# Kernel tuning notes

Hardware: AMD Instinct MI355X
Metric: run time of the kernel (lower is better)

Reference implementation:

```python
import jax, jax.numpy as jnp
import numpy as np

K = 5          # k = min(5, min(S, T)) with S = T = 4096
SIGMA = 1.0
EPS_VAR = 1e-08
EPS_LOG = 1e-08


def _entropy(p):
    # sum(-p * log2(clamp(p, 1e-8)), axis=1).mean()
    return jnp.sum(-p * jnp.log2(jnp.clip(p, EPS_LOG, None)), axis=1).mean()


def _pairwise_dist(x):
    # Euclidean cdist via GEMM (matches torch's use_mm_for_euclid path)
    sq = jnp.sum(x * x, axis=1)                       # [N]
    d2 = sq[:, None] + sq[None, :] - 2.0 * (x @ x.T)  # [N, N]
    d2 = jnp.maximum(d2, 0.0)
    # safe sqrt (zero diagonal) — value identical, grad-safe
    return jnp.where(d2 > 0, jnp.sqrt(jnp.where(d2 > 0, d2, 1.0)), 0.0)


def _row_var(block):
    # sqrt(k-th smallest distance per row + eps): max of k smallest
    kth = -jax.lax.top_k(-block, K)[0][:, -1]
    return jnp.sqrt(kth + EPS_VAR)                    # [rows]


def _sim(block, var_row, zero_diag):
    s = jnp.exp(-block / (2.0 * (var_row[:, None] * SIGMA) ** 2))
    if zero_diag:
        n = block.shape[0]
        s = s * (1.0 - jnp.eye(n, dtype=s.dtype))
    return s


def _forward(Feature_all, logit_all, y_source):
    S = y_source.shape[0]
    logit_source = logit_all[:S]
    logit_target = logit_all[S:]

    # cross-entropy on source
    logp = jax.nn.log_softmax(logit_source, axis=1)
    loss_cl = -jnp.take_along_axis(logp, y_source[:, None], axis=1).mean()

    # entropy of target softmax
    loss_ce = _entropy(jax.nn.softmax(logit_target, axis=1))

    # reg_loss_dist
    dist = _pairwise_dist(Feature_all)                # [N, N]
    d_ss = dist[:S, :S]
    d_st = dist[:S, S:]
    d_tt = dist[S:, S:]
    d_ts = dist[S:, :S]

    sim_ss = _sim(d_ss, _row_var(d_ss), True)
    sim_st = _sim(d_st, _row_var(d_st), False)
    sim_tt = _sim(d_tt, _row_var(d_tt), True)
    sim_ts = _sim(d_ts, _row_var(d_ts), False)

    src_intra = jnp.max(sim_ss, axis=1)
    src_inter = jnp.max(sim_st, axis=1)
    tgt_intra = jnp.max(sim_tt, axis=1)
    tgt_inter = jnp.max(sim_ts, axis=1)

    loss_reg = (jnp.abs(src_intra - src_inter).mean()
                + jnp.abs(tgt_intra - tgt_inter).mean())
    return loss_cl, loss_ce, loss_reg


def setup_inputs() -> dict:
    key = jax.random.key(0)
    k1, k2, k3 = jax.random.split(key, 3)
    N, D, C, S = 8192, 256, 65, 4096
    return {
        "Feature_all": jax.random.normal(k1, (N, D), dtype=jnp.float32),
        "logit_all": jax.random.normal(k2, (N, C), dtype=jnp.float32),
        "y_source": jax.random.randint(k3, (S,), 0, C, dtype=jnp.int64
                                       if jax.config.jax_enable_x64 else jnp.int32),
        "device": 0,
    }


def reference(Feature_all, logit_all, y_source, device):
    del device  # torch-specific, ignored
    return _forward(Feature_all, logit_all, y_source)
```

## Files before the change

### kernel.cpp

```cpp
#include <hip/hip_runtime.h>
#include <stdint.h>

#define Nn 8192
#define Dd 256
#define Ss 4096
#define Cc 65

#define TI 128
#define TJ 128
#define BK 32
#define CHUNK 256
#define NCHUNK (Nn / CHUNK)
#define NJT (CHUNK / TJ)
#define KS (Dd / BK)
#define NL (NCHUNK * 2)

#define BIGF 3.0e37f

typedef float f4 __attribute__((ext_vector_type(4)));
typedef __bf16 bf8 __attribute__((ext_vector_type(8)));

__device__ __forceinline__ float wredsum(float v) {
#pragma unroll
  for (int o = 32; o; o >>= 1) v += __shfl_xor(v, o, 64);
  return v;
}
__device__ __forceinline__ float wredmax(float v) {
#pragma unroll
  for (int o = 32; o; o >>= 1) v = fmaxf(v, __shfl_xor(v, o, 64));
  return v;
}

__device__ __forceinline__ unsigned short f2bf(float f) {
  unsigned int u = __float_as_uint(f);
  u = (u + 0x7fffu + ((u >> 16) & 1u)) >> 16;
  return (unsigned short)u;
}

__global__ __launch_bounds__(256) void prep_kernel(const float* __restrict__ X,
                                                   unsigned short* __restrict__ xb,
                                                   float* __restrict__ sqn) {
  int row = blockIdx.x * 4 + (threadIdx.x >> 6);
  int lane = threadIdx.x & 63;
  f4 v = ((const f4*)(X + (size_t)row * Dd))[lane];
  float ss = v[0] * v[0] + v[1] * v[1] + v[2] * v[2] + v[3] * v[3];
  ss = wredsum(ss);
  if (lane == 0) sqn[row] = ss;
  ushort4 o;
  o.x = f2bf(v[0]); o.y = f2bf(v[1]); o.z = f2bf(v[2]); o.w = f2bf(v[3]);
  ((ushort4*)(xb + (size_t)row * Dd))[lane] = o;
}

__device__ __forceinline__ void stage16(const void* g, void* l) {
  __builtin_amdgcn_global_load_lds((__attribute__((address_space(1))) void*)g,
                                   (__attribute__((address_space(3))) void*)l, 16, 0, 0);
}

__global__ __launch_bounds__(256) void dist_kernel(const unsigned short* __restrict__ xb,
                                                   const float* __restrict__ sqn,
                                                   float* __restrict__ top5ws) {
  __shared__ unsigned short ldsA[2][TJ * BK];
  __shared__ unsigned short ldsB[2][TI * BK];

  const int tid = threadIdx.x;
  const int lane = tid & 63;
  const int wv = tid >> 6;
  const int q = lane >> 4;
  const int c = lane & 15;
  const int jw = wv & 1;
  const int iw = wv >> 1;

  const int ib = (blockIdx.x / NCHUNK) * TI;
  const int chunk = blockIdx.x % NCHUNK;
  const int jc0 = chunk * CHUNK;

  const int swz = q ^ ((lane >> 1) & 3);
  const int pr = lane >> 2;
  const int qd = (lane & 3) ^ ((lane >> 3) & 3);
  const int u0 = wv * 2, u1 = wv * 2 + 1;
  const int gcol = qd * 8;

  float top[4][5];
#pragma unroll
  for (int a = 0; a < 4; ++a)
#pragma unroll
    for (int b = 0; b < 5; ++b) top[a][b] = BIGF;

  const int iwbase = ib + iw * 64;

  for (int jt = 0; jt < NJT; ++jt) {
    const int jb = jc0 + jt * TJ;

    f4 acc[4][4];
    f4 z = {0.f, 0.f, 0.f, 0.f};
#pragma unroll
    for (int a = 0; a < 4; ++a)
#pragma unroll
      for (int b2 = 0; b2 < 4; ++b2) acc[a][b2] = z;

    stage16(xb + (size_t)(jb + u0 * 16 + pr) * Dd + gcol, &ldsA[0][u0 * 512]);
    stage16(xb + (size_t)(jb + u1 * 16 + pr) * Dd + gcol, &ldsA[0][u1 * 512]);
    stage16(xb + (size_t)(ib + u0 * 16 + pr) * Dd + gcol, &ldsB[0][u0 * 512]);
    stage16(xb + (size_t)(ib + u1 * 16 + pr) * Dd + gcol, &ldsB[0][u1 * 512]);
    __syncthreads();

#pragma unroll
    for (int ks = 0; ks < KS; ++ks) {
      const int b = ks & 1;
      if (ks + 1 < KS) {
        const int k0 = (ks + 1) * BK;
        stage16(xb + (size_t)(jb + u0 * 16 + pr) * Dd + k0 + gcol, &ldsA[b ^ 1][u0 * 512]);
        stage16(xb + (size_t)(jb + u1 * 16 + pr) * Dd + k0 + gcol, &ldsA[b ^ 1][u1 * 512]);
        stage16(xb + (size_t)(ib + u0 * 16 + pr) * Dd + k0 + gcol, &ldsB[b ^ 1][u0 * 512]);
        stage16(xb + (size_t)(ib + u1 * 16 + pr) * Dd + k0 + gcol, &ldsB[b ^ 1][u1 * 512]);
      }
      bf8 aF[4], bF[4];
#pragma unroll
      for (int rt = 0; rt < 4; ++rt)
        aF[rt] = *(const bf8*)&ldsA[b][(jw * 64 + rt * 16 + c) * 32 + swz * 8];
#pragma unroll
      for (int ct = 0; ct < 4; ++ct)
        bF[ct] = *(const bf8*)&ldsB[b][(iw * 64 + ct * 16 + c) * 32 + swz * 8];
#pragma unroll
      for (int rt = 0; rt < 4; ++rt)
#pragma unroll
        for (int ct = 0; ct < 4; ++ct)
          acc[rt][ct] = __builtin_amdgcn_mfma_f32_16x16x32_bf16(aF[rt], bF[ct], acc[rt][ct], 0, 0, 0);
      __syncthreads();
    }

    const int jrow = jb + jw * 64;
    f4 sq4[4];
#pragma unroll
    for (int rt = 0; rt < 4; ++rt) sq4[rt] = *(const f4*)&sqn[jrow + rt * 16 + q * 4];
    const bool mayDiag = (jrow == iwbase);
#pragma unroll
    for (int ct = 0; ct < 4; ++ct) {
      float t[16];
#pragma unroll
      for (int rt = 0; rt < 4; ++rt)
#pragma unroll
        for (int r = 0; r < 4; ++r)
          t[rt * 4 + r] = fmaf(acc[rt][ct][r], -2.0f, sq4[rt][r]);
      if (mayDiag && ((c >> 2) == q)) t[ct * 4 + (c & 3)] = BIGF;
      float tm = fminf(fminf(fminf(fminf(t[0], t[1]), fminf(t[2], t[3])),
                             fminf(fminf(t[4], t[5]), fminf(t[6], t[7]))),
                       fminf(fminf(fminf(t[8], t[9]), fminf(t[10], t[11])),
                             fminf(fminf(t[12], t[13]), fminf(t[14], t[15]))));
      if (tm < top[ct][4]) {
#pragma unroll
        for (int kk = 0; kk < 16; ++kk) {
          float x = t[kk];
          if (x < top[ct][4]) {
#pragma unroll
            for (int s = 0; s < 4; ++s) {
              float lo = fminf(top[ct][s], x);
              x = fmaxf(top[ct][s], x);
              top[ct][s] = lo;
            }
            top[ct][4] = x;
          }
        }
      }
    }
  }

  const int list = chunk * 2 + jw;
#pragma unroll
  for (int ct = 0; ct < 4; ++ct) {
    float a0 = top[ct][0], a1 = top[ct][1], a2 = top[ct][2], a3 = top[ct][3], a4 = top[ct][4];
#pragma unroll
    for (int off = 16; off <= 32; off <<= 1) {
      float b0 = __shfl_xor(a0, off, 64);
      float b1 = __shfl_xor(a1, off, 64);
      float b2 = __shfl_xor(a2, off, 64);
      float b3 = __shfl_xor(a3, off, 64);
      float b4 = __shfl_xor(a4, off, 64);
      float c0 = fminf(a0, b0);
      float c1 = fminf(fminf(a1, b1), fmaxf(a0, b0));
      float c2 = fminf(fminf(a2, b2), fminf(fmaxf(a1, b0), fmaxf(a0, b1)));
      float c3 = fminf(fminf(a3, b3), fminf(fmaxf(a2, b0), fminf(fmaxf(a1, b1), fmaxf(a0, b2))));
      float c4 = fminf(fminf(a4, b4),
                       fminf(fmaxf(a3, b0),
                             fminf(fmaxf(a2, b1), fminf(fmaxf(a1, b2), fmaxf(a0, b3)))));
      a0 = c0; a1 = c1; a2 = c2; a3 = c3; a4 = c4;
    }
    if (q == 0) {
      int i = iwbase + ct * 16 + c;
      top5ws[(size_t)(list * 5 + 0) * Nn + i] = a0;
      top5ws[(size_t)(list * 5 + 1) * Nn + i] = a1;
      top5ws[(size_t)(list * 5 + 2) * Nn + i] = a2;
      top5ws[(size_t)(list * 5 + 3) * Nn + i] = a3;
      top5ws[(size_t)(list * 5 + 4) * Nn + i] = a4;
    }
  }
}

__device__ __forceinline__ void merge5(const float* a, const float* b, float* o) {
  float t0 = fminf(a[0], b[0]);
  float t1 = fminf(fminf(a[1], b[1]), fmaxf(a[0], b[0]));
  float t2 = fminf(fminf(a[2], b[2]), fminf(fmaxf(a[1], b[0]), fmaxf(a[0], b[1])));
  float t3 = fminf(fminf(a[3], b[3]), fminf(fmaxf(a[2], b[0]), fminf(fmaxf(a[1], b[1]), fmaxf(a[0], b[2]))));
  float t4 = fminf(fminf(a[4], b[4]),
                   fminf(fmaxf(a[3], b[0]),
                         fminf(fmaxf(a[2], b[1]), fminf(fmaxf(a[1], b[2]), fmaxf(a[0], b[3])))));
  o[0] = t0; o[1] = t1; o[2] = t2; o[3] = t3; o[4] = t4;
}

__global__ __launch_bounds__(256) void tail_kernel(const float* __restrict__ logit,
                                                   const int* __restrict__ y,
                                                   const float* __restrict__ top5ws,
                                                   const float* __restrict__ sqn,
                                                   float* __restrict__ part_cl,
                                                   float* __restrict__ part_ce,
                                                   float* __restrict__ part_reg) {
  __shared__ float red[256];
  const int bx = blockIdx.x;
  if (bx < 2048) {
    int row = bx * 4 + (threadIdx.x >> 6);
    int lane = threadIdx.x & 63;
    const float* xr = logit + (size_t)row * Cc;
    float x1 = xr[lane];
    float x2 = (lane == 0) ? xr[64] : -BIGF;
    float mx = wredmax(fmaxf(x1, x2));
    float e1 = expf(x1 - mx);
    float e2 = (lane == 0) ? expf(x2 - mx) : 0.f;
    float Z = wredsum(e1 + e2);
    float res;
    if (row < Ss) {
      int yy = y[row];
      float pick = (lane == yy ? x1 : 0.f) + ((lane == 0 && yy == 64) ? x2 : 0.f);
      float xy = wredsum(pick);
      res = -(xy - mx - logf(Z));
    } else {
      float p1 = e1 / Z;
      float t1 = -p1 * log2f(fmaxf(p1, 1e-8f));
      if (lane == 0) {
        float p2 = e2 / Z;
        t1 += -p2 * log2f(fmaxf(p2, 1e-8f));
      }
      res = wredsum(t1);
    }
    __shared__ float a4[4];
    if (lane == 0) a4[threadIdx.x >> 6] = res;
    __syncthreads();
    if (threadIdx.x == 0) {
      float s = a4[0] + a4[1] + a4[2] + a4[3];
      if (bx < 1024) part_cl[bx] = s;
      else part_ce[bx - 1024] = s;
    }
  } else {
    int i = (bx - 2048) * 256 + threadIdx.x;
    float mm[2][5];
#pragma unroll
    for (int h = 0; h < 2; ++h) {
      float run[5];
      int L0 = h * 32;
#pragma unroll 4
      for (int k = 0; k < 32; ++k) {
        float lv[5];
#pragma unroll
        for (int s = 0; s < 5; ++s) lv[s] = top5ws[(size_t)((L0 + k) * 5 + s) * Nn + i];
        if (k == 0) {
#pragma unroll
          for (int s = 0; s < 5; ++s) run[s] = lv[s];
        } else {
          merge5(run, lv, run);
        }
      }
#pragma unroll
      for (int s = 0; s < 5; ++s) mm[h][s] = run[s];
    }
    bool srcRow = (i < Ss);
    int hin = srcRow ? 0 : 1, hout = srcRow ? 1 : 0;
    float A0 = mm[hin][0];
    float A3 = mm[hin][3];
    float B0 = mm[hout][0];
    float B4 = mm[hout][4];
    float sq = sqn[i];
    float dmin_a = sqrtf(fmaxf(A0 + sq, 0.f));
    float kth_a = sqrtf(fmaxf(A3 + sq, 0.f));
    float dmin_b = sqrtf(fmaxf(B0 + sq, 0.f));
    float kth_b = sqrtf(fmaxf(B4 + sq, 0.f));
    float sa = expf(-dmin_a / (2.f * (kth_a + 1e-8f)));
    float sb = expf(-dmin_b / (2.f * (kth_b + 1e-8f)));
    float v = fabsf(sa - sb);
    red[threadIdx.x] = v;
    __syncthreads();
#pragma unroll
    for (int s = 128; s; s >>= 1) {
      if (threadIdx.x < s) red[threadIdx.x] += red[threadIdx.x + s];
      __syncthreads();
    }
    if (threadIdx.x == 0) part_reg[bx - 2048] = red[0];
  }
}

__global__ __launch_bounds__(256) void final_kernel(const float* __restrict__ part_cl,
                                                    const float* __restrict__ part_ce,
                                                    const float* __restrict__ part_reg,
                                                    float* __restrict__ out) {
  __shared__ double red[256];
  int tid = threadIdx.x;
  double a = 0.0;
  for (int k = tid; k < 1024; k += 256) a += (double)part_cl[k];
  red[tid] = a; __syncthreads();
  for (int s = 128; s; s >>= 1) { if (tid < s) red[tid] += red[tid + s]; __syncthreads(); }
  double cl = red[0]; __syncthreads();
  a = 0.0;
  for (int k = tid; k < 1024; k += 256) a += (double)part_ce[k];
  red[tid] = a; __syncthreads();
  for (int s = 128; s; s >>= 1) { if (tid < s) red[tid] += red[tid + s]; __syncthreads(); }
  double ce = red[0]; __syncthreads();
  a = (tid < 32) ? (double)part_reg[tid] : 0.0;
  red[tid] = a; __syncthreads();
  for (int s = 128; s; s >>= 1) { if (tid < s) red[tid] += red[tid + s]; __syncthreads(); }
  if (tid == 0) {
    out[0] = (float)(cl / 4096.0);
    out[1] = (float)(ce / 4096.0);
    out[2] = (float)(red[0] / 4096.0);
  }
}

extern "C" void kernel_launch(void* const* d_in, const int* in_sizes, int n_in,
                              void* d_out, int out_size, void* d_ws, size_t ws_size,
                              hipStream_t stream) {
  (void)in_sizes; (void)n_in; (void)out_size; (void)ws_size;
  const float* X = (const float*)d_in[0];
  const float* logit = (const float*)d_in[1];
  const int* y = (const int*)d_in[2];
  float* out = (float*)d_out;
  char* ws = (char*)d_ws;

  unsigned short* xb = (unsigned short*)ws;
  float* sqn = (float*)(ws + (4u << 20));
  float* top5 = (float*)(ws + (4u << 20) + (64u << 10));
  float* part_cl = (float*)(ws + (16u << 20));
  float* part_ce = part_cl + 1024;
  float* part_reg = part_ce + 1024;

  hipLaunchKernelGGL(prep_kernel, dim3(2048), dim3(256), 0, stream, X, xb, sqn);
  hipLaunchKernelGGL(dist_kernel, dim3((Nn / TI) * NCHUNK), dim3(256), 0, stream, xb, sqn, top5);
  hipLaunchKernelGGL(tail_kernel, dim3(2048 + 32), dim3(256), 0, stream,
                     logit, y, top5, sqn, part_cl, part_ce, part_reg);
  hipLaunchKernelGGL(final_kernel, dim3(1), dim3(256), 0, stream, part_cl, part_ce, part_reg, out);
}
```

Measured before the change: 169.0 us.

## Keep full-K i-tile resident in LDS, stream j-tile from global, drop final kernel

The distance kernel now loads the whole 128x256 i-row tile into LDS once per block and widens each block's j-chunk from 256 to 1024 columns. The j-side operands are read straight from global memory into registers with a one-step prefetch, which removes the per-k-step LDS staging and barriers. The tail kernel merges fewer partial top-5 lists, and the final reduction kernel is replaced by atomicAdd into a zeroed output. In exchange there are fewer blocks, uncoalesced direct global loads for A, and float atomics that make the summation order nondeterministic.

```diff
diff --git a/kernel.cpp b/kernel.cpp
--- a/kernel.cpp
+++ b/kernel.cpp
@@ -8,12 +8,10 @@
 
 #define TI 128
 #define TJ 128
-#define BK 32
-#define CHUNK 256
+#define CHUNK 1024
 #define NCHUNK (Nn / CHUNK)
 #define NJT (CHUNK / TJ)
-#define KS (Dd / BK)
-#define NL (NCHUNK * 2)
+#define KS 8
 
 #define BIGF 3.0e37f
 
@@ -56,11 +54,10 @@
                                    (__attribute__((address_space(3))) void*)l, 16, 0, 0);
 }
 
-__global__ __launch_bounds__(256) void dist_kernel(const unsigned short* __restrict__ xb,
-                                                   const float* __restrict__ sqn,
-                                                   float* __restrict__ top5ws) {
-  __shared__ unsigned short ldsA[2][TJ * BK];
-  __shared__ unsigned short ldsB[2][TI * BK];
+__global__ __launch_bounds__(256, 2) void dist_kernel(const unsigned short* __restrict__ xb,
+                                                      const float* __restrict__ sqn,
+                                                      float* __restrict__ top5ws) {
+  __shared__ unsigned short ldsB[KS][TI * 32];
 
   const int tid = threadIdx.x;
   const int lane = tid & 63;
@@ -70,15 +67,24 @@
   const int jw = wv & 1;
   const int iw = wv >> 1;
 
-  const int ib = (blockIdx.x / NCHUNK) * TI;
-  const int chunk = blockIdx.x % NCHUNK;
+  const int it = blockIdx.x & 63;
+  const int chunk = blockIdx.x >> 6;
+  const int ib = it * TI;
   const int jc0 = chunk * CHUNK;
 
   const int swz = q ^ ((lane >> 1) & 3);
   const int pr = lane >> 2;
   const int qd = (lane & 3) ^ ((lane >> 3) & 3);
-  const int u0 = wv * 2, u1 = wv * 2 + 1;
-  const int gcol = qd * 8;
+
+#pragma unroll
+  for (int it2 = 0; it2 < 16; ++it2) {
+    int idx = wv * 16 + it2;
+    int rg = idx & 7;
+    int s = idx >> 3;
+    stage16(xb + (size_t)(ib + rg * 16 + pr) * Dd + s * 32 + qd * 8,
+            &ldsB[s][rg * 512]);
+  }
+  __syncthreads();
 
   float top[4][5];
 #pragma unroll
@@ -87,9 +93,11 @@
     for (int b = 0; b < 5; ++b) top[a][b] = BIGF;
 
   const int iwbase = ib + iw * 64;
+  const unsigned short* Ab = xb + (size_t)(jw * 64 + c) * Dd + q * 8;
 
   for (int jt = 0; jt < NJT; ++jt) {
     const int jb = jc0 + jt * TJ;
+    const unsigned short* Aj = Ab + (size_t)jb * Dd;
 
     f4 acc[4][4];
     f4 z = {0.f, 0.f, 0.f, 0.f};
@@ -98,35 +106,34 @@
 #pragma unroll
       for (int b2 = 0; b2 < 4; ++b2) acc[a][b2] = z;
 
-    stage16(xb + (size_t)(jb + u0 * 16 + pr) * Dd + gcol, &ldsA[0][u0 * 512]);
-    stage16(xb + (size_t)(jb + u1 * 16 + pr) * Dd + gcol, &ldsA[0][u1 * 512]);
-    stage16(xb + (size_t)(ib + u0 * 16 + pr) * Dd + gcol, &ldsB[0][u0 * 512]);
-    stage16(xb + (size_t)(ib + u1 * 16 + pr) * Dd + gcol, &ldsB[0][u1 * 512]);
-    __syncthreads();
+    bf8 aC[4], bC[4], aN[4], bN[4];
+#pragma unroll
+    for (int rt = 0; rt < 4; ++rt) aC[rt] = *(const bf8*)(Aj + rt * 16 * Dd);
+#pragma unroll
+    for (int ct = 0; ct < 4; ++ct)
+      bC[ct] = *(const bf8*)&ldsB[0][(iw * 64 + ct * 16 + c) * 32 + swz * 8];
 
 #pragma unroll
     for (int ks = 0; ks < KS; ++ks) {
-      const int b = ks & 1;
       if (ks + 1 < KS) {
-        const int k0 = (ks + 1) * BK;
-        stage16(xb + (size_t)(jb + u0 * 16 + pr) * Dd + k0 + gcol, &ldsA[b ^ 1][u0 * 512]);
-        stage16(xb + (size_t)(jb + u1 * 16 + pr) * Dd + k0 + gcol, &ldsA[b ^ 1][u1 * 512]);
-        stage16(xb + (size_t)(ib + u0 * 16 + pr) * Dd + k0 + gcol, &ldsB[b ^ 1][u0 * 512]);
-        stage16(xb + (size_t)(ib + u1 * 16 + pr) * Dd + k0 + gcol, &ldsB[b ^ 1][u1 * 512]);
-      }
-      bf8 aF[4], bF[4];
+#pragma unroll
+        for (int rt = 0; rt < 4; ++rt)
+          aN[rt] = *(const bf8*)(Aj + rt * 16 * Dd + (ks + 1) * 32);
+#pragma unroll
+        for (int ct = 0; ct < 4; ++ct)
+          bN[ct] = *(const bf8*)&ldsB[ks + 1][(iw * 64 + ct * 16 + c) * 32 + swz * 8];
+      }
 #pragma unroll
       for (int rt = 0; rt < 4; ++rt)
-        aF[rt] = *(const bf8*)&ldsA[b][(jw * 64 + rt * 16 + c) * 32 + swz * 8];
-#pragma unroll
-      for (int ct = 0; ct < 4; ++ct)
-        bF[ct] = *(const bf8*)&ldsB[b][(iw * 64 + ct * 16 + c) * 32 + swz * 8];
-#pragma unroll
-      for (int rt = 0; rt < 4; ++rt)
 #pragma unroll
         for (int ct = 0; ct < 4; ++ct)
-          acc[rt][ct] = __builtin_amdgcn_mfma_f32_16x16x32_bf16(aF[rt], bF[ct], acc[rt][ct], 0, 0, 0);
-      __syncthreads();
+          acc[rt][ct] = __builtin_amdgcn_mfma_f32_16x16x32_bf16(aC[rt], bC[ct], acc[rt][ct], 0, 0, 0);
+      if (ks + 1 < KS) {
+#pragma unroll
+        for (int rt = 0; rt < 4; ++rt) aC[rt] = aN[rt];
+#pragma unroll
+        for (int ct = 0; ct < 4; ++ct) bC[ct] = bN[ct];
+      }
     }
 
     const int jrow = jb + jw * 64;
@@ -211,9 +218,7 @@
                                                    const int* __restrict__ y,
                                                    const float* __restrict__ top5ws,
                                                    const float* __restrict__ sqn,
-                                                   float* __restrict__ part_cl,
-                                                   float* __restrict__ part_ce,
-                                                   float* __restrict__ part_reg) {
+                                                   float* __restrict__ out) {
   __shared__ float red[256];
   const int bx = blockIdx.x;
   if (bx < 2048) {
@@ -245,9 +250,8 @@
     if (lane == 0) a4[threadIdx.x >> 6] = res;
     __syncthreads();
     if (threadIdx.x == 0) {
-      float s = a4[0] + a4[1] + a4[2] + a4[3];
-      if (bx < 1024) part_cl[bx] = s;
-      else part_ce[bx - 1024] = s;
+      float s = (a4[0] + a4[1] + a4[2] + a4[3]) * (1.0f / 4096.0f);
+      atomicAdd(&out[bx < 1024 ? 0 : 1], s);
     }
   } else {
     int i = (bx - 2048) * 256 + threadIdx.x;
@@ -255,9 +259,9 @@
 #pragma unroll
     for (int h = 0; h < 2; ++h) {
       float run[5];
-      int L0 = h * 32;
-#pragma unroll 4
-      for (int k = 0; k < 32; ++k) {
+      int L0 = h * 8;
+#pragma unroll
+      for (int k = 0; k < 8; ++k) {
         float lv[5];
 #pragma unroll
         for (int s = 0; s < 5; ++s) lv[s] = top5ws[(size_t)((L0 + k) * 5 + s) * Nn + i];
@@ -292,40 +296,14 @@
       if (threadIdx.x < s) red[threadIdx.x] += red[threadIdx.x + s];
       __syncthreads();
     }
-    if (threadIdx.x == 0) part_reg[bx - 2048] = red[0];
-  }
-}
-
-__global__ __launch_bounds__(256) void final_kernel(const float* __restrict__ part_cl,
-                                                    const float* __restrict__ part_ce,
-                                                    const float* __restrict__ part_reg,
-                                                    float* __restrict__ out) {
-  __shared__ double red[256];
-  int tid = threadIdx.x;
-  double a = 0.0;
-  for (int k = tid; k < 1024; k += 256) a += (double)part_cl[k];
-  red[tid] = a; __syncthreads();
-  for (int s = 128; s; s >>= 1) { if (tid < s) red[tid] += red[tid + s]; __syncthreads(); }
-  double cl = red[0]; __syncthreads();
-  a = 0.0;
-  for (int k = tid; k < 1024; k += 256) a += (double)part_ce[k];
-  red[tid] = a; __syncthreads();
-  for (int s = 128; s; s >>= 1) { if (tid < s) red[tid] += red[tid + s]; __syncthreads(); }
-  double ce = red[0]; __syncthreads();
-  a = (tid < 32) ? (double)part_reg[tid] : 0.0;
-  red[tid] = a; __syncthreads();
-  for (int s = 128; s; s >>= 1) { if (tid < s) red[tid] += red[tid + s]; __syncthreads(); }
-  if (tid == 0) {
-    out[0] = (float)(cl / 4096.0);
-    out[1] = (float)(ce / 4096.0);
-    out[2] = (float)(red[0] / 4096.0);
+    if (threadIdx.x == 0) atomicAdd(&out[2], red[0] * (1.0f / 4096.0f));
   }
 }
 
 extern "C" void kernel_launch(void* const* d_in, const int* in_sizes, int n_in,
                               void* d_out, int out_size, void* d_ws, size_t ws_size,
                               hipStream_t stream) {
-  (void)in_sizes; (void)n_in; (void)out_size; (void)ws_size;
+  (void)in_sizes; (void)n_in; (void)ws_size;
   const float* X = (const float*)d_in[0];
   const float* logit = (const float*)d_in[1];
   const int* y = (const int*)d_in[2];
@@ -335,13 +313,9 @@
   unsigned short* xb = (unsigned short*)ws;
   float* sqn = (float*)(ws + (4u << 20));
   float* top5 = (float*)(ws + (4u << 20) + (64u << 10));
-  float* part_cl = (float*)(ws + (16u << 20));
-  float* part_ce = part_cl + 1024;
-  float* part_reg = part_ce + 1024;
-
+
+  hipMemsetAsync(d_out, 0, (size_t)out_size * 4, stream);
   hipLaunchKernelGGL(prep_kernel, dim3(2048), dim3(256), 0, stream, X, xb, sqn);
   hipLaunchKernelGGL(dist_kernel, dim3((Nn / TI) * NCHUNK), dim3(256), 0, stream, xb, sqn, top5);
-  hipLaunchKernelGGL(tail_kernel, dim3(2048 + 32), dim3(256), 0, stream,
-                     logit, y, top5, sqn, part_cl, part_ce, part_reg);
-  hipLaunchKernelGGL(final_kernel, dim3(1), dim3(256), 0, stream, part_cl, part_ce, part_reg, out);
-}
+  hipLaunchKernelGGL(tail_kernel, dim3(2048 + 32), dim3(256), 0, stream, logit, y, top5, sqn, out);
+}
```

Result: slower. 181.8 us (+7.6%).
